# Kernel tuning notes

Measured on AMD Instinct MI355X. Metric: run time of the kernel, lower is better.

The kernel has to match this reference:

```python
import jax, jax.numpy as jnp
import numpy as np
import math

D_MODEL = 1024
N_HEADS = 16
D_K = D_MODEL // N_HEADS  # 64


def setup_inputs() -> dict:
    key = jax.random.key(0)
    ks = jax.random.split(key, 12)
    B, S = 2, 2048
    scale = 1.0 / math.sqrt(D_MODEL)
    inp = {
        'q': jax.random.normal(ks[0], (B, S, D_MODEL), jnp.float32),
        'k': jax.random.normal(ks[1], (B, S, D_MODEL), jnp.float32),
        'v': jax.random.normal(ks[2], (B, S, D_MODEL), jnp.float32),
        'Wq': jax.random.normal(ks[3], (D_MODEL, D_MODEL), jnp.float32) * scale,
        'bq': jnp.zeros((D_MODEL,), jnp.float32),
        'Wk': jax.random.normal(ks[4], (D_MODEL, D_MODEL), jnp.float32) * scale,
        'bk': jnp.zeros((D_MODEL,), jnp.float32),
        'Wv': jax.random.normal(ks[5], (D_MODEL, D_MODEL), jnp.float32) * scale,
        'bv': jnp.zeros((D_MODEL,), jnp.float32),
        'Wo': jax.random.normal(ks[6], (D_MODEL, D_MODEL), jnp.float32) * scale,
        'bo': jnp.zeros((D_MODEL,), jnp.float32),
        'phase': jax.random.normal(ks[7], (N_HEADS, 1, 1), jnp.float32),
    }
    return inp


def _split_heads(x, B):
    # (B, S, D) -> (B, H, S, d_k)
    return x.reshape(B, -1, N_HEADS, D_K).transpose(0, 2, 1, 3)


def _phase_sync(x, phase):
    # x: (B, H, S, d_k); treat [first half, second half] as complex pair,
    # rotate by per-head phase: (re + i*im) * exp(i*phase)
    half = D_K // 2
    xr, xi = x[..., :half], x[..., half:]
    c = jnp.cos(phase)[None]  # (1, H, 1, 1)
    s = jnp.sin(phase)[None]
    return jnp.concatenate([xr * c - xi * s, xr * s + xi * c], axis=-1)


def reference(q, k, v, Wq, bq, Wk, bk, Wv, bv, Wo, bo, phase):
    B = q.shape[0]
    qh = _split_heads(q @ Wq.T + bq, B)
    kh = _split_heads(k @ Wk.T + bk, B)
    vh = _split_heads(v @ Wv.T + bv, B)
    qh = _phase_sync(qh, phase)
    kh = _phase_sync(kh, phase)
    scores = jnp.einsum('bhqd,bhkd->bhqk', qh, kh) / math.sqrt(D_K)
    attn = jax.nn.softmax(scores, axis=-1)  # dropout is identity in eval
    out = jnp.einsum('bhqk,bhkd->bhqd', attn, vh)
    out = out.transpose(0, 2, 1, 3).reshape(B, -1, D_MODEL)
    return out @ Wo.T + bo
```

## Files before the change

kernel.cpp:

```cpp
#include <hip/hip_runtime.h>
#include <hip/hip_bf16.h>


typedef short bf16x8 __attribute__((ext_vector_type(8)));
typedef float f32x4 __attribute__((ext_vector_type(4)));
typedef unsigned short u16;
typedef unsigned short u16x8 __attribute__((ext_vector_type(8)));
typedef unsigned short u16x4 __attribute__((ext_vector_type(4)));

static __device__ __forceinline__ u16 f2bf(float x) {
    __hip_bfloat16 b = __float2bfloat16(x);
    return *reinterpret_cast<u16*>(&b);
}
static __device__ __forceinline__ bf16x8 g8(const u16* p) {
    return *reinterpret_cast<const bf16x8*>(p);
}
static __device__ __forceinline__ float fast_exp2(float x) {
#if __has_builtin(__builtin_amdgcn_exp2f)
    return __builtin_amdgcn_exp2f(x);
#else
    return exp2f(x);
#endif
}
static __device__ __forceinline__ void gl16(const u16* g, u16* l) {
    __builtin_amdgcn_global_load_lds(
        (const __attribute__((address_space(1))) void*)g,
        (__attribute__((address_space(3))) void*)l, 16, 0, 0);
}
static __device__ __forceinline__ u16x8 cvt8(const float4& a, const float4& b) {
    u16x8 r;
    r[0] = f2bf(a.x); r[1] = f2bf(a.y); r[2] = f2bf(a.z); r[3] = f2bf(a.w);
    r[4] = f2bf(b.x); r[5] = f2bf(b.y); r[6] = f2bf(b.z); r[7] = f2bf(b.w);
    return r;
}

#define SWZ(row, col) ((row) * 32 + ((col) ^ ((((row) >> 1) & 3) << 3)))

__global__ void k_splitW(const float* __restrict__ w0, const float* __restrict__ w1,
                         const float* __restrict__ w2, const float* __restrict__ w3,
                         u16* __restrict__ h0, u16* __restrict__ h1,
                         u16* __restrict__ h2, u16* __restrict__ h3) {
    const int i = blockIdx.x * 256 + threadIdx.x;
    const float* s;
    u16* H;
    if (blockIdx.y == 0) { s = w0; H = h0; }
    else if (blockIdx.y == 1) { s = w1; H = h1; }
    else if (blockIdx.y == 2) { s = w2; H = h2; }
    else { s = w3; H = h3; }
    float4 val = reinterpret_cast<const float4*>(s)[i];
    u16x4 h;
    h[0] = f2bf(val.x); h[1] = f2bf(val.y);
    h[2] = f2bf(val.z); h[3] = f2bf(val.w);
    reinterpret_cast<u16x4*>(H)[i] = h;
}

__global__ __launch_bounds__(256) void k_gemm(
    const float* __restrict__ qf, const float* __restrict__ kf,
    const float* __restrict__ vf,
    const u16* __restrict__ Wqh, const u16* __restrict__ Wkh,
    const u16* __restrict__ Wvh,
    const float* __restrict__ bq, const float* __restrict__ bk,
    const float* __restrict__ bv_,
    const float* __restrict__ phase,
    u16* __restrict__ Qrh, u16* __restrict__ Krh,
    u16* __restrict__ VTh) {
    __shared__ __attribute__((aligned(16))) u16 sA0[128 * 32];
    __shared__ __attribute__((aligned(16))) u16 sA1[128 * 32];
    __shared__ __attribute__((aligned(16))) u16 sB0[128 * 32];
    __shared__ __attribute__((aligned(16))) u16 sB1[128 * 32];

    const int z = blockIdx.z;
    const float* Af;
    const u16* Bh;
    const float* bias;
    if (z == 0) { Af = qf; Bh = Wqh; bias = bq; }
    else if (z == 1) { Af = kf; Bh = Wkh; bias = bk; }
    else { Af = vf; Bh = Wvh; bias = bv_; }

    const int flat = blockIdx.y * 8 + blockIdx.x;
    const int tau = (flat & 7) * 32 + (flat >> 3);
    const int bx = tau & 7, by = tau >> 3;

    const int t = threadIdx.x;
    const int l = t & 63, w = t >> 6;
    const int wr = w >> 1, wc = w & 1;
    const int m0 = by * 128, n0 = bx * 128;
    const int fr = l & 15;
    const int fk = (l >> 4) * 8;
    const int ar = wr * 64 + fr;
    const int br = wc * 64 + fr;

    const int grow = w * 32 + (l >> 2);
    const int colx = ((l & 3) * 8) ^ (((grow >> 1) & 3) << 3);
    const int lb0 = (w * 2) * 512, lb1 = (w * 2 + 1) * 512;
    const u16* pB0 = Bh + (size_t)(n0 + grow) * 1024 + colx;
    const u16* pB1 = Bh + (size_t)(n0 + grow + 16) * 1024 + colx;

    const int srow = t >> 2;
    const int scol = (t & 3) * 8;
    const float* pA0 = Af + (size_t)(m0 + srow) * 1024 + scol;
    const float* pA1 = Af + (size_t)(m0 + 64 + srow) * 1024 + scol;
    const int so0 = SWZ(srow, scol);
    const int so1 = SWZ(srow + 64, scol);

    float4 a00, a01, a10, a11;
    auto loadA = [&](int kk) {
        const int ko = kk * 32;
        a00 = *reinterpret_cast<const float4*>(pA0 + ko);
        a01 = *reinterpret_cast<const float4*>(pA0 + ko + 4);
        a10 = *reinterpret_cast<const float4*>(pA1 + ko);
        a11 = *reinterpret_cast<const float4*>(pA1 + ko + 4);
    };
    auto stageB = [&](u16* SB, int kk) {
        const int ko = kk * 32;
        gl16(pB0 + ko, &SB[lb0]);
        gl16(pB1 + ko, &SB[lb1]);
    };
    auto writeA = [&](u16* SA) {
        *reinterpret_cast<u16x8*>(&SA[so0]) = cvt8(a00, a01);
        *reinterpret_cast<u16x8*>(&SA[so1]) = cvt8(a10, a11);
    };

    f32x4 acc[4][4];
#pragma unroll
    for (int m = 0; m < 4; ++m)
#pragma unroll
        for (int n = 0; n < 4; ++n) acc[m][n] = (f32x4){0.f, 0.f, 0.f, 0.f};

    auto compute = [&](const u16* SA, const u16* SB) {
        bf16x8 fa[4], fb[4];
#pragma unroll
        for (int m = 0; m < 4; ++m)
            fa[m] = *reinterpret_cast<const bf16x8*>(&SA[SWZ(ar + m * 16, fk)]);
#pragma unroll
        for (int n = 0; n < 4; ++n)
            fb[n] = *reinterpret_cast<const bf16x8*>(&SB[SWZ(br + n * 16, fk)]);
#pragma unroll
        for (int m = 0; m < 4; ++m)
#pragma unroll
            for (int n = 0; n < 4; ++n)
                acc[m][n] = __builtin_amdgcn_mfma_f32_16x16x32_bf16(fa[m], fb[n], acc[m][n], 0, 0, 0);
    };

    loadA(0);
    stageB(sB0, 0);
    writeA(sA0);
    __syncthreads();

    for (int kk = 0; kk < 32; kk += 2) {
        loadA(kk + 1);
        stageB(sB1, kk + 1);
        compute(sA0, sB0);
        writeA(sA1);
        __syncthreads();
        const bool more = (kk + 2 < 32);
        if (more) {
            loadA(kk + 2);
            stageB(sB0, kk + 2);
        }
        compute(sA1, sB1);
        if (more) writeA(sA0);
        __syncthreads();
    }

    const int er4 = (l >> 4) * 4;
    float bvv[4];
#pragma unroll
    for (int n = 0; n < 4; ++n) bvv[n] = bias[n0 + wc * 64 + n * 16 + fr];

    if (z == 2) {
#pragma unroll
        for (int m = 0; m < 4; ++m) {
            const int row0 = m0 + wr * 64 + m * 16 + er4;
            const int bb = row0 >> 11;
            const int ss = row0 & 2047;
#pragma unroll
            for (int n = 0; n < 4; ++n) {
                const int col = n0 + wc * 64 + n * 16 + fr;
                const int hh_ = col >> 6, dd = col & 63;
                u16x4 vv;
#pragma unroll
                for (int r = 0; r < 4; ++r) vv[r] = f2bf(acc[m][n][r] + bvv[n]);
                *reinterpret_cast<u16x4*>(
                    &VTh[((size_t)(bb * 16 + hh_) * 64 + dd) * 2048 + ss]) = vv;
            }
        }
    } else {
        u16* Dh = z ? Krh : Qrh;
        const float sc = z ? 1.0f : 0.18033688011112042f;
        const int head = bx * 2 + wc;
        float sv, cv;
        sincosf(phase[head], &sv, &cv);
#pragma unroll
        for (int m = 0; m < 4; ++m)
#pragma unroll
            for (int n = 0; n < 2; ++n) {
#pragma unroll
                for (int r = 0; r < 4; ++r) {
                    const float xr = acc[m][n][r] + bvv[n];
                    const float xi = acc[m][n + 2][r] + bvv[n + 2];
                    const float o0 = (xr * cv - xi * sv) * sc;
                    const float o1 = (xr * sv + xi * cv) * sc;
                    const int row = m0 + wr * 64 + m * 16 + er4 + r;
                    const size_t i0 = (size_t)row * 1024 + head * 64 + n * 16 + fr;
                    Dh[i0] = f2bf(o0);
                    Dh[i0 + 32] = f2bf(o1);
                }
            }
    }
}

__global__ __launch_bounds__(256) void k_gemm1(
    const u16* __restrict__ Ah, const u16* __restrict__ Bh,
    const float* __restrict__ bias, float* __restrict__ C) {
    __shared__ __attribute__((aligned(16))) u16 sA0[128 * 32];
    __shared__ __attribute__((aligned(16))) u16 sA1[128 * 32];
    __shared__ __attribute__((aligned(16))) u16 sB0[128 * 32];
    __shared__ __attribute__((aligned(16))) u16 sB1[128 * 32];

    const int flat = blockIdx.y * 8 + blockIdx.x;
    const int tau = (flat & 7) * 32 + (flat >> 3);
    const int bx = tau & 7, by = tau >> 3;

    const int t = threadIdx.x;
    const int l = t & 63, w = t >> 6;
    const int wr = w >> 1, wc = w & 1;
    const int m0 = by * 128, n0 = bx * 128;
    const int fr = l & 15;
    const int fk = (l >> 4) * 8;
    const int ar = wr * 64 + fr;
    const int br = wc * 64 + fr;

    const int grow = w * 32 + (l >> 2);
    const int colx = ((l & 3) * 8) ^ (((grow >> 1) & 3) << 3);
    const int lb0 = (w * 2) * 512, lb1 = (w * 2 + 1) * 512;
    const u16* pA0 = Ah + (size_t)(m0 + grow) * 1024 + colx;
    const u16* pA1 = Ah + (size_t)(m0 + grow + 16) * 1024 + colx;
    const u16* pB0 = Bh + (size_t)(n0 + grow) * 1024 + colx;
    const u16* pB1 = Bh + (size_t)(n0 + grow + 16) * 1024 + colx;

    auto stage = [&](u16* SA, u16* SB, int kk) {
        const int ko = kk * 32;
        gl16(pA0 + ko, &SA[lb0]);
        gl16(pA1 + ko, &SA[lb1]);
        gl16(pB0 + ko, &SB[lb0]);
        gl16(pB1 + ko, &SB[lb1]);
    };

    f32x4 acc[4][4];
#pragma unroll
    for (int m = 0; m < 4; ++m)
#pragma unroll
        for (int n = 0; n < 4; ++n) acc[m][n] = (f32x4){0.f, 0.f, 0.f, 0.f};

    auto compute = [&](const u16* SA, const u16* SB) {
        bf16x8 fa[4], fb[4];
#pragma unroll
        for (int m = 0; m < 4; ++m)
            fa[m] = *reinterpret_cast<const bf16x8*>(&SA[SWZ(ar + m * 16, fk)]);
#pragma unroll
        for (int n = 0; n < 4; ++n)
            fb[n] = *reinterpret_cast<const bf16x8*>(&SB[SWZ(br + n * 16, fk)]);
#pragma unroll
        for (int m = 0; m < 4; ++m)
#pragma unroll
            for (int n = 0; n < 4; ++n)
                acc[m][n] = __builtin_amdgcn_mfma_f32_16x16x32_bf16(fa[m], fb[n], acc[m][n], 0, 0, 0);
    };

    stage(sA0, sB0, 0);
    __syncthreads();
    for (int kk = 0; kk < 32; kk += 2) {
        stage(sA1, sB1, kk + 1);
        compute(sA0, sB0);
        __syncthreads();
        if (kk + 2 < 32) stage(sA0, sB0, kk + 2);
        compute(sA1, sB1);
        __syncthreads();
    }

    const int er4 = (l >> 4) * 4;
    float bvv[4];
#pragma unroll
    for (int n = 0; n < 4; ++n) bvv[n] = bias[n0 + wc * 64 + n * 16 + fr];
#pragma unroll
    for (int m = 0; m < 4; ++m)
#pragma unroll
        for (int n = 0; n < 4; ++n) {
            const int col = n0 + wc * 64 + n * 16 + fr;
            const size_t rb = (size_t)(m0 + wr * 64 + m * 16 + er4) * 1024 + col;
#pragma unroll
            for (int r = 0; r < 4; ++r) C[rb + (size_t)r * 1024] = acc[m][n][r] + bvv[n];
        }
}

#define SM_M2 17.312340490667562f

#define ATTN_TILE(SK, SV)                                                      \
  {                                                                            \
    f32x4 s[2][4];                                                             \
    _Pragma("unroll") for (int qm = 0; qm < 2; ++qm)                           \
      _Pragma("unroll") for (int n = 0; n < 4; ++n)                            \
        s[qm][n] = (f32x4){-SM_M2, -SM_M2, -SM_M2, -SM_M2};                    \
    _Pragma("unroll") for (int n = 0; n < 4; ++n)                              \
      _Pragma("unroll") for (int ks = 0; ks < 2; ++ks) {                       \
        bf16x8 bkh = *reinterpret_cast<const bf16x8*>(                         \
            &SK[(n * 16 + fr) * 64 + ((ks * 32 + fk) ^ rswz)]);                \
        _Pragma("unroll") for (int qm = 0; qm < 2; ++qm)                       \
          s[qm][n] = __builtin_amdgcn_mfma_f32_16x16x32_bf16(aqh[qm][ks], bkh, s[qm][n], 0, 0, 0); \
      }                                                                        \
    _Pragma("unroll") for (int qm = 0; qm < 2; ++qm)                           \
      _Pragma("unroll") for (int n = 0; n < 4; ++n)                            \
        _Pragma("unroll") for (int r = 0; r < 4; ++r) {                        \
          const float p = fast_exp2(s[qm][n][r]);                              \
          const int prow = w * 32 + qm * 16 + (l >> 4) * 4 + r;                \
          const int pcol = (n * 16 + (l & 15)) ^ ((prow & 7) << 3);            \
          sPh[prow * 64 + pcol] = f2bf(p);                                     \
        }                                                                      \
    bf16x8 bph[2][2];                                                          \
    _Pragma("unroll") for (int qm = 0; qm < 2; ++qm)                           \
      _Pragma("unroll") for (int ks = 0; ks < 2; ++ks)                         \
        bph[qm][ks] = *reinterpret_cast<const bf16x8*>(                        \
            &sPh[(w * 32 + qm * 16 + fr) * 64 + ((ks * 32 + fk) ^ rswz)]);     \
    _Pragma("unroll") for (int m = 0; m < 4; ++m)                              \
      _Pragma("unroll") for (int ks = 0; ks < 2; ++ks) {                       \
        bf16x8 avh = *reinterpret_cast<const bf16x8*>(                         \
            &SV[(m * 16 + fr) * 64 + ((ks * 32 + fk) ^ rswz)]);                \
        _Pragma("unroll") for (int qm = 0; qm < 2; ++qm)                       \
          aco[qm][m] = __builtin_amdgcn_mfma_f32_16x16x32_bf16(avh, bph[qm][ks], aco[qm][m], 0, 0, 0); \
      }                                                                        \
    _Pragma("unroll") for (int qm = 0; qm < 2; ++qm)                           \
      _Pragma("unroll") for (int ks = 0; ks < 2; ++ks)                         \
        acl[qm] = __builtin_amdgcn_mfma_f32_16x16x32_bf16(vone, bph[qm][ks], acl[qm], 0, 0, 0); \
  }

#define ATTN_STAGE(SK, SV)                                                     \
  {                                                                            \
    _Pragma("unroll") for (int i = 0; i < 2; ++i) {                            \
      *reinterpret_cast<bf16x8*>(&SK[soff[i]]) = rKh[i];                       \
      *reinterpret_cast<bf16x8*>(&SV[soff[i]]) = rVh[i];                       \
    }                                                                          \
  }

__global__ __launch_bounds__(256) void k_attn(
    const u16* __restrict__ Qh,
    const u16* __restrict__ Kh,
    const u16* __restrict__ VTh,
    u16* __restrict__ AOh) {
    __shared__ __attribute__((aligned(16))) u16 sK0[4096];
    __shared__ __attribute__((aligned(16))) u16 sK1[4096];
    __shared__ __attribute__((aligned(16))) u16 sV0[4096];
    __shared__ __attribute__((aligned(16))) u16 sV1[4096];
    __shared__ __attribute__((aligned(16))) u16 sPh[128 * 64];

    const int t = threadIdx.x;
    const int l = t & 63, w = t >> 6;
    const int flat = blockIdx.y * 16 + blockIdx.x;
    const int tau = (flat & 7) * 64 + (flat >> 3);
    const int q0 = (tau & 15) * 128;
    const int bh = tau >> 4;
    const int b = bh >> 4, h = bh & 15;
    const size_t qrow0 = (size_t)b * 2048 + q0;

    const u16* Qb_h = Qh + qrow0 * 1024 + h * 64;
    const u16* Kb_h = Kh + (size_t)b * 2048 * 1024 + h * 64;
    const u16* Vb_h = VTh + (size_t)bh * 64 * 2048;

    const int fr = l & 15;
    const int fk = (l >> 4) * 8;

    bf16x8 aqh[2][2];
#pragma unroll
    for (int qm = 0; qm < 2; ++qm)
#pragma unroll
        for (int ks = 0; ks < 2; ++ks) {
            const size_t qo = (size_t)(w * 32 + qm * 16 + fr) * 1024 + ks * 32 + fk;
            aqh[qm][ks] = g8(Qb_h + qo);
        }

    bf16x8 vone;
#pragma unroll
    for (int j = 0; j < 8; ++j) vone[j] = (short)0x3F80;

    f32x4 aco[2][4];
    f32x4 acl[2];
#pragma unroll
    for (int qm = 0; qm < 2; ++qm) {
        acl[qm] = (f32x4){0.f, 0.f, 0.f, 0.f};
#pragma unroll
        for (int m = 0; m < 4; ++m) aco[qm][m] = (f32x4){0.f, 0.f, 0.f, 0.f};
    }

    const int sr = t >> 3, sc = (t & 7) * 8;
    bf16x8 rKh[2], rVh[2];
    auto load_kv = [&](int tt) {
        const int kv0 = tt * 64;
#pragma unroll
        for (int i = 0; i < 2; ++i) {
            const int r2 = sr + i * 32;
            rKh[i] = g8(Kb_h + (size_t)(kv0 + r2) * 1024 + sc);
            rVh[i] = g8(Vb_h + (size_t)r2 * 2048 + kv0 + sc);
        }
    };
    int soff[2];
#pragma unroll
    for (int i = 0; i < 2; ++i) {
        const int r2 = sr + i * 32;
        soff[i] = r2 * 64 + (sc ^ ((r2 & 7) << 3));
    }
    const int rswz = (fr & 7) << 3;

    load_kv(0);
    ATTN_STAGE(sK0, sV0);
    __syncthreads();

    for (int tt = 0; tt < 32; tt += 2) {
        load_kv(tt + 1);
        ATTN_TILE(sK0, sV0);
        ATTN_STAGE(sK1, sV1);
        __syncthreads();
        if (tt + 2 < 32) load_kv(tt + 2);
        ATTN_TILE(sK1, sV1);
        if (tt + 2 < 32) ATTN_STAGE(sK0, sV0);
        __syncthreads();
    }

#pragma unroll
    for (int qm = 0; qm < 2; ++qm) {
        const float inv = 1.0f / acl[qm][0];
#pragma unroll
        for (int m = 0; m < 4; ++m) aco[qm][m] *= inv;
    }

    float* Ol = reinterpret_cast<float*>(
        (w == 0) ? sK0 : (w == 1) ? sK1 : (w == 2) ? sV0 : sV1);
#pragma unroll
    for (int qm = 0; qm < 2; ++qm) {
        const int qr = qm * 16 + (l & 15);
        const int sw = (qr & 7) << 3;
#pragma unroll
        for (int m = 0; m < 4; ++m)
#pragma unroll
            for (int r = 0; r < 4; ++r)
                Ol[qr * 64 + ((m * 16 + (l >> 4) * 4 + r) ^ sw)] = aco[qm][m][r];
    }
#pragma unroll
    for (int it = 0; it < 4; ++it) {
        const int qr = (l >> 3) + it * 8;
        const int cb = (l & 7) * 8;
        const int sw = (qr & 7) << 3;
        const float* srcp = &Ol[qr * 64 + (cb ^ sw)];
        u16x8 oh;
#pragma unroll
        for (int j = 0; j < 8; ++j) oh[j] = f2bf(srcp[j]);
        const size_t ob = (qrow0 + w * 32 + qr) * 1024 + h * 64 + cb;
        *reinterpret_cast<u16x8*>(&AOh[ob]) = oh;
    }
}

extern "C" void kernel_launch(void* const* d_in, const int* in_sizes, int n_in,
                              void* d_out, int out_size, void* d_ws, size_t ws_size,
                              hipStream_t stream) {
    const float* q = (const float*)d_in[0];
    const float* k = (const float*)d_in[1];
    const float* v = (const float*)d_in[2];
    const float* Wq = (const float*)d_in[3];
    const float* bq = (const float*)d_in[4];
    const float* Wk = (const float*)d_in[5];
    const float* bk = (const float*)d_in[6];
    const float* Wv = (const float*)d_in[7];
    const float* bv = (const float*)d_in[8];
    const float* Wo = (const float*)d_in[9];
    const float* bo = (const float*)d_in[10];
    const float* phase = (const float*)d_in[11];
    float* out = (float*)d_out;

    char* ws = (char*)d_ws;
    const size_t MB = 1u << 20;
    u16* Wq_h = (u16*)(ws + 0 * MB);
    u16* Wk_h = (u16*)(ws + 2 * MB);
    u16* Wv_h = (u16*)(ws + 4 * MB);
    u16* Wo_h = (u16*)(ws + 6 * MB);
    u16* QR_h = (u16*)(ws + 64 * MB);
    u16* KR_h = (u16*)(ws + 80 * MB);
    u16* VT_h = (u16*)(ws + 96 * MB);
    u16* AO_h = (u16*)(ws + 16 * MB);

    k_splitW<<<dim3(1024, 4), 256, 0, stream>>>(Wq, Wk, Wv, Wo,
                                                Wq_h, Wk_h, Wv_h, Wo_h);
    k_gemm<<<dim3(8, 32, 3), 256, 0, stream>>>(
        q, k, v, Wq_h, Wk_h, Wv_h,
        bq, bk, bv, phase, QR_h, KR_h, VT_h);
    k_attn<<<dim3(16, 32), 256, 0, stream>>>(QR_h, KR_h, VT_h, AO_h);
    k_gemm1<<<dim3(8, 32), 256, 0, stream>>>(AO_h, Wo_h, bo, out);
    (void)in_sizes; (void)n_in; (void)out_size; (void)ws_size;
}
```

Measured before the change: 124.4 us.

## Deepen GEMM prefetch pipeline with explicit vmcnt waits and sched barriers

Rewrites the main loops of the QKV projection and output projection GEMMs to keep two K-tiles of global loads in flight. It replaces __syncthreads with hand-placed s_waitcnt vmcnt(N)/s_barrier pairs and sched_barrier fences, so later loads are not drained at every barrier. In the QKV kernel the fp32 A tiles are double-buffered in registers (two sets) so the load runs one more stage ahead. This costs extra VGPRs and relies on exact vmcnt counting for correctness.

```diff
diff --git a/kernel.cpp b/kernel.cpp
--- a/kernel.cpp
+++ b/kernel.cpp
@@ -35,6 +35,15 @@
 }
 
 #define SWZ(row, col) ((row) * 32 + ((col) ^ ((((row) >> 1) & 3) << 3)))
+
+#define SBAR0 __builtin_amdgcn_sched_barrier(0)
+#define WAITBAR(N)                                                             \
+    {                                                                          \
+        asm volatile("s_waitcnt vmcnt(" #N ") lgkmcnt(0)" ::: "memory");       \
+        SBAR0;                                                                 \
+        __builtin_amdgcn_s_barrier();                                          \
+        SBAR0;                                                                 \
+    }
 
 __global__ void k_splitW(const float* __restrict__ w0, const float* __restrict__ w1,
                          const float* __restrict__ w2, const float* __restrict__ w3,
@@ -92,34 +101,46 @@
 
     const int grow = w * 32 + (l >> 2);
     const int colx = ((l & 3) * 8) ^ (((grow >> 1) & 3) << 3);
-    const int lb0 = (w * 2) * 512, lb1 = (w * 2 + 1) * 512;
+    const int lb0 = w * 1024, lb1 = w * 1024 + 512;
     const u16* pB0 = Bh + (size_t)(n0 + grow) * 1024 + colx;
     const u16* pB1 = Bh + (size_t)(n0 + grow + 16) * 1024 + colx;
 
     const int srow = t >> 2;
     const int scol = (t & 3) * 8;
-    const float* pA0 = Af + (size_t)(m0 + srow) * 1024 + scol;
-    const float* pA1 = Af + (size_t)(m0 + 64 + srow) * 1024 + scol;
+    const float* pAr0 = Af + (size_t)(m0 + srow) * 1024 + scol;
+    const float* pAr1 = Af + (size_t)(m0 + 64 + srow) * 1024 + scol;
     const int so0 = SWZ(srow, scol);
     const int so1 = SWZ(srow + 64, scol);
 
-    float4 a00, a01, a10, a11;
-    auto loadA = [&](int kk) {
+    float4 ra0_0, ra0_1, ra0_2, ra0_3;
+    float4 ra1_0, ra1_1, ra1_2, ra1_3;
+    auto loadA0 = [&](int kk) {
         const int ko = kk * 32;
-        a00 = *reinterpret_cast<const float4*>(pA0 + ko);
-        a01 = *reinterpret_cast<const float4*>(pA0 + ko + 4);
-        a10 = *reinterpret_cast<const float4*>(pA1 + ko);
-        a11 = *reinterpret_cast<const float4*>(pA1 + ko + 4);
+        ra0_0 = *reinterpret_cast<const float4*>(pAr0 + ko);
+        ra0_1 = *reinterpret_cast<const float4*>(pAr0 + ko + 4);
+        ra0_2 = *reinterpret_cast<const float4*>(pAr1 + ko);
+        ra0_3 = *reinterpret_cast<const float4*>(pAr1 + ko + 4);
+    };
+    auto loadA1 = [&](int kk) {
+        const int ko = kk * 32;
+        ra1_0 = *reinterpret_cast<const float4*>(pAr0 + ko);
+        ra1_1 = *reinterpret_cast<const float4*>(pAr0 + ko + 4);
+        ra1_2 = *reinterpret_cast<const float4*>(pAr1 + ko);
+        ra1_3 = *reinterpret_cast<const float4*>(pAr1 + ko + 4);
+    };
+    auto writeA0 = [&](u16* SA) {
+        *reinterpret_cast<u16x8*>(&SA[so0]) = cvt8(ra0_0, ra0_1);
+        *reinterpret_cast<u16x8*>(&SA[so1]) = cvt8(ra0_2, ra0_3);
+    };
+    auto writeA1 = [&](u16* SA) {
+        *reinterpret_cast<u16x8*>(&SA[so0]) = cvt8(ra1_0, ra1_1);
+        *reinterpret_cast<u16x8*>(&SA[so1]) = cvt8(ra1_2, ra1_3);
     };
     auto stageB = [&](u16* SB, int kk) {
         const int ko = kk * 32;
         gl16(pB0 + ko, &SB[lb0]);
         gl16(pB1 + ko, &SB[lb1]);
     };
-    auto writeA = [&](u16* SA) {
-        *reinterpret_cast<u16x8*>(&SA[so0]) = cvt8(a00, a01);
-        *reinterpret_cast<u16x8*>(&SA[so1]) = cvt8(a10, a11);
-    };
 
     f32x4 acc[4][4];
 #pragma unroll
@@ -142,25 +163,37 @@
                 acc[m][n] = __builtin_amdgcn_mfma_f32_16x16x32_bf16(fa[m], fb[n], acc[m][n], 0, 0, 0);
     };
 
-    loadA(0);
     stageB(sB0, 0);
-    writeA(sA0);
-    __syncthreads();
+    SBAR0;
+    loadA0(0);
+    loadA1(1);
+    writeA0(sA0);
+    asm volatile("s_waitcnt vmcnt(0) lgkmcnt(0)" ::: "memory");
+    SBAR0;
+    __builtin_amdgcn_s_barrier();
+    SBAR0;
 
     for (int kk = 0; kk < 32; kk += 2) {
-        loadA(kk + 1);
         stageB(sB1, kk + 1);
+        SBAR0;
+        if (kk + 2 < 32) loadA0(kk + 2);
         compute(sA0, sB0);
-        writeA(sA1);
-        __syncthreads();
-        const bool more = (kk + 2 < 32);
-        if (more) {
-            loadA(kk + 2);
-            stageB(sB0, kk + 2);
-        }
+        writeA1(sA1);
+        if (kk + 2 < 32) {
+            WAITBAR(4)
+        } else {
+            WAITBAR(0)
+        }
+        if (kk + 2 < 32) stageB(sB0, kk + 2);
+        SBAR0;
+        if (kk + 3 < 32) loadA1(kk + 3);
         compute(sA1, sB1);
-        if (more) writeA(sA0);
-        __syncthreads();
+        if (kk + 2 < 32) writeA0(sA0);
+        if (kk + 3 < 32) {
+            WAITBAR(4)
+        } else {
+            WAITBAR(0)
+        }
     }
 
     const int er4 = (l >> 4) * 4;
@@ -233,7 +266,7 @@
 
     const int grow = w * 32 + (l >> 2);
     const int colx = ((l & 3) * 8) ^ (((grow >> 1) & 3) << 3);
-    const int lb0 = (w * 2) * 512, lb1 = (w * 2 + 1) * 512;
+    const int lb0 = w * 1024, lb1 = w * 1024 + 512;
     const u16* pA0 = Ah + (size_t)(m0 + grow) * 1024 + colx;
     const u16* pA1 = Ah + (size_t)(m0 + grow + 16) * 1024 + colx;
     const u16* pB0 = Bh + (size_t)(n0 + grow) * 1024 + colx;
@@ -269,14 +302,34 @@
     };
 
     stage(sA0, sB0, 0);
-    __syncthreads();
+    SBAR0;
+    stage(sA1, sB1, 1);
+    asm volatile("s_waitcnt vmcnt(4) lgkmcnt(0)" ::: "memory");
+    SBAR0;
+    __builtin_amdgcn_s_barrier();
+    SBAR0;
+
     for (int kk = 0; kk < 32; kk += 2) {
-        stage(sA1, sB1, kk + 1);
         compute(sA0, sB0);
-        __syncthreads();
-        if (kk + 2 < 32) stage(sA0, sB0, kk + 2);
+        SBAR0;
+        __builtin_amdgcn_s_barrier();
+        SBAR0;
+        if (kk + 2 < 32) {
+            stage(sA0, sB0, kk + 2);
+            WAITBAR(4)
+        } else {
+            WAITBAR(0)
+        }
         compute(sA1, sB1);
-        __syncthreads();
+        SBAR0;
+        __builtin_amdgcn_s_barrier();
+        SBAR0;
+        if (kk + 3 < 32) {
+            stage(sA1, sB1, kk + 3);
+            WAITBAR(4)
+        } else {
+            WAITBAR(0)
+        }
     }
 
     const int er4 = (l >> 4) * 4;
```

Result: slower. 131.0 us (+5.3%).
